# Performance work log

Measured on AMD Instinct MI355X. Metric: run time of the kernel, lower is better.

The kernel has to match this reference:

```python
import jax, jax.numpy as jnp
import numpy as np

T = 2048          # tokens (flattened batch*seq, vLLM style)
HID = 2048        # hidden_size
NH = 16           # num_heads
D_NOPE = 128
D_ROPE = 64
D_QK = D_NOPE + D_ROPE   # 192
D_V = 128
Q_LORA = 1536
KV_LORA = 512
THETA = 10000.0
EPS = 1e-6
SCALING = D_QK ** -0.5


def _rmsnorm(x, g):
    return x * jax.lax.rsqrt(jnp.mean(x * x, axis=-1, keepdims=True) + EPS) * g


def _rope(pos, x):
    # interleaved (is_neox_style=False) rotary embedding
    d = x.shape[-1]
    inv = 1.0 / (THETA ** (jnp.arange(0, d, 2, dtype=jnp.float32) / d))
    f = pos.astype(jnp.float32)[:, None] * inv          # [T, d/2]
    cos, sin = jnp.cos(f), jnp.sin(f)
    for _ in range(x.ndim - 2):                          # broadcast over heads
        cos, sin = cos[:, None], sin[:, None]
    x1, x2 = x[..., 0::2], x[..., 1::2]
    o1 = x1 * cos - x2 * sin
    o2 = x1 * sin + x2 * cos
    return jnp.stack([o1, o2], axis=-1).reshape(x.shape)


def setup_inputs() -> dict:
    key = jax.random.key(0)
    ks = jax.random.split(key, 6)
    s = 0.02
    return {
        "hidden_states": jax.random.normal(ks[0], (T, HID), jnp.float32),
        "positions": jnp.arange(T, dtype=jnp.int32),
        "w_qkv_a": jax.random.normal(ks[1], (HID, Q_LORA + KV_LORA + D_ROPE), jnp.float32) * s,
        "g_q": jnp.ones((Q_LORA,), jnp.float32),
        "w_q_b": jax.random.normal(ks[2], (Q_LORA, NH * D_QK), jnp.float32) * s,
        "g_kv": jnp.ones((KV_LORA,), jnp.float32),
        "w_kv_b": jax.random.normal(ks[3], (KV_LORA, NH * (D_NOPE + D_V)), jnp.float32) * s,
        "w_o": jax.random.normal(ks[4], (NH * D_V, HID), jnp.float32) * s,
    }


def reference(hidden_states, positions, w_qkv_a, g_q, w_q_b, g_kv, w_kv_b, w_o):
    # fused low-rank a-projection: [T, q_lora + kv_lora + rope]
    qkv_a = hidden_states @ w_qkv_a
    q_lat = qkv_a[:, :Q_LORA]
    kv_lat = qkv_a[:, Q_LORA:Q_LORA + KV_LORA]
    k_pe = qkv_a[:, Q_LORA + KV_LORA:]                   # [T, rope]

    # query path: rmsnorm -> b-projection -> [T, H, d_qk]
    q = (_rmsnorm(q_lat, g_q) @ w_q_b).reshape(T, NH, D_QK)
    q_nope, q_pe = q[..., :D_NOPE], q[..., D_NOPE:]

    # kv path: rmsnorm -> b-projection -> [T, H, nope + v]
    kv = (_rmsnorm(kv_lat, g_kv) @ w_kv_b).reshape(T, NH, D_NOPE + D_V)
    k_nope, v = kv[..., :D_NOPE], kv[..., D_NOPE:]

    q_pe = _rope(positions, q_pe)                        # [T, H, rope]
    k_pe = _rope(positions, k_pe)                        # [T, rope] shared MQA rope key

    qf = jnp.concatenate([q_nope, q_pe], axis=-1)        # [T, H, d_qk]
    kf = jnp.concatenate([k_nope, jnp.broadcast_to(k_pe[:, None, :], (T, NH, D_ROPE))], axis=-1)

    scores = jnp.einsum("thd,shd->hts", qf, kf) * SCALING   # [H, T, T]
    mask = jnp.tril(jnp.ones((T, T), dtype=bool))
    scores = jnp.where(mask, scores, jnp.finfo(scores.dtype).min)
    probs = jax.nn.softmax(scores, axis=-1)
    out = jnp.einsum("hts,shd->thd", probs, v)           # [T, H, d_v]
    return out.reshape(T, NH * D_V) @ w_o                # [T, hidden]
```

## Files before the change

### kernel.cpp

```cpp
#include <hip/hip_runtime.h>
#include <hip/hip_bf16.h>
#include <math.h>

typedef __bf16 bf16_t;
typedef __bf16 bf16x8 __attribute__((ext_vector_type(8)));
typedef float floatx4 __attribute__((ext_vector_type(4)));
typedef int intx4 __attribute__((ext_vector_type(4)));

#define T_TOK 2048
#define HID 2048
#define NH 16
#define D_NOPE 128
#define D_ROPE 64
#define D_QK 192
#define D_V 128
#define Q_LORA 1536
#define KV_LORA 512
#define QKV_N 2112
#define QKV_NPAD 2176
#define SCALING 0.07216878364870323f
#define LOG2E 1.442695041f
#define EXP_C1 (SCALING * LOG2E)
#define EXP_C2 (12.0f * LOG2E)

#define MFMA_BF16(a, b, c) __builtin_amdgcn_mfma_f32_16x16x32_bf16(a, b, c, 0, 0, 0)

__device__ __forceinline__ void gload16(const void* g, void* l) {
    __builtin_amdgcn_global_load_lds(
        (const __attribute__((address_space(1))) unsigned int*)g,
        (__attribute__((address_space(3))) unsigned int*)l, 16, 0, 0);
}

template <int MODE>
__device__ __forceinline__ void gemm_body(
    const bf16_t* __restrict__ A, const bf16_t* __restrict__ Bt,
    float* __restrict__ Cf, bf16_t* __restrict__ Cb,
    bf16_t* __restrict__ kfull, bf16_t* __restrict__ vT,
    float* __restrict__ sqq, float* __restrict__ sqkv,
    int N, int K, int Ast, int Bst, int m0, int n0, bf16_t* S)
{
    bf16_t* As = S;
    bf16_t* Bs = S + 16384;
    const int tid = threadIdx.x;
    const int lane = tid & 63;
    const int w = tid >> 6;
    const int wm = w >> 1, wn = w & 1;
    const int l15 = lane & 15, quad = lane >> 4;
    const int ckey = (l15 >> 1) & 3;

    floatx4 acc[4][4] = {};

#define GSTAGE(db_, k0_)                                                                 \
    do {                                                                                 \
        _Pragma("unroll")                                                                \
        for (int it = 0; it < 4; ++it) {                                                 \
            int slot = it * 256 + tid;                                                   \
            int kk2 = slot >> 9;                                                         \
            int r = (slot >> 2) & 127;                                                   \
            int c = slot & 3;                                                            \
            int cs = c ^ ((r >> 1) & 3);                                                 \
            gload16((const char*)(A + (size_t)(m0 + r) * Ast + (k0_) + kk2 * 32 + cs * 8),\
                    (char*)(As + (size_t)(db_)*8192) + slot * 16);                       \
            gload16((const char*)(Bt + (size_t)(n0 + r) * Bst + (k0_) + kk2 * 32 + cs * 8),\
                    (char*)(Bs + (size_t)(db_)*8192) + slot * 16);                       \
        }                                                                                \
    } while (0)

    GSTAGE(0, 0);
    int db = 0;
    for (int k0 = 0; k0 < K; k0 += 64) {
        __syncthreads();
        if (k0 + 64 < K) GSTAGE(db ^ 1, k0 + 64);
        const bf16_t* Ab = As + (size_t)db * 8192;
        const bf16_t* Bb = Bs + (size_t)db * 8192;
#pragma unroll
        for (int kk2 = 0; kk2 < 2; ++kk2) {
            bf16x8 af[4], bfr[4];
#pragma unroll
            for (int mi = 0; mi < 4; ++mi)
                af[mi] = *(const bf16x8*)(Ab + kk2 * 4096 +
                                          (wm * 64 + mi * 16 + l15) * 32 +
                                          (quad ^ ckey) * 8);
#pragma unroll
            for (int ni = 0; ni < 4; ++ni)
                bfr[ni] = *(const bf16x8*)(Bb + kk2 * 4096 +
                                           (wn * 64 + ni * 16 + l15) * 32 +
                                           (quad ^ ckey) * 8);
#pragma unroll
            for (int mi = 0; mi < 4; ++mi)
#pragma unroll
                for (int ni = 0; ni < 4; ++ni)
                    acc[mi][ni] = MFMA_BF16(af[mi], bfr[ni], acc[mi][ni]);
        }
        db ^= 1;
    }
#undef GSTAGE

    if (MODE == 3) {
#pragma unroll
        for (int mi = 0; mi < 4; ++mi)
#pragma unroll
            for (int ni = 0; ni < 4; ++ni)
#pragma unroll
                for (int r = 0; r < 4; ++r) {
                    int row = m0 + wm * 64 + mi * 16 + quad * 4 + r;
                    int col = n0 + wn * 64 + ni * 16 + l15;
                    Cb[(size_t)row * N + col] = (bf16_t)acc[mi][ni][r];
                }
        float* sq = (n0 + 128 <= Q_LORA) ? sqq
                  : ((n0 >= Q_LORA && n0 + 128 <= Q_LORA + KV_LORA) ? sqkv : nullptr);
        if (sq) {
#pragma unroll
            for (int mi = 0; mi < 4; ++mi)
#pragma unroll
                for (int r = 0; r < 4; ++r) {
                    float s = 0.f;
#pragma unroll
                    for (int ni = 0; ni < 4; ++ni) {
                        float v = acc[mi][ni][r]; s += v * v;
                    }
                    s += __shfl_xor(s, 1); s += __shfl_xor(s, 2);
                    s += __shfl_xor(s, 4); s += __shfl_xor(s, 8);
                    if (l15 == 0)
                        atomicAdd(&sq[m0 + wm * 64 + mi * 16 + quad * 4 + r], s);
                }
        }
        return;
    }

    if (MODE == 1) {
#pragma unroll
        for (int mi = 0; mi < 4; ++mi)
#pragma unroll
            for (int r = 0; r < 4; ++r) {
                int row = m0 + wm * 64 + mi * 16 + quad * 4 + r;
                float rq = rsqrtf(sqq[row] * (1.f / Q_LORA) + 1e-6f);
#pragma unroll
                for (int ni = 0; ni < 4; ++ni) {
                    int col = n0 + wn * 64 + ni * 16 + l15;
                    Cb[(size_t)row * N + col] = (bf16_t)(acc[mi][ni][r] * rq);
                }
            }
        return;
    }

    if (MODE == 2) {
        const int hh = n0 >> 8;
        if ((n0 & 255) == 0) {
#pragma unroll
            for (int mi = 0; mi < 4; ++mi)
#pragma unroll
                for (int r = 0; r < 4; ++r) {
                    int row = m0 + wm * 64 + mi * 16 + quad * 4 + r;
                    float rkv = rsqrtf(sqkv[row] * (1.f / KV_LORA) + 1e-6f);
#pragma unroll
                    for (int ni = 0; ni < 4; ++ni) {
                        int dd = wn * 64 + ni * 16 + l15;
                        kfull[((size_t)hh * T_TOK + row) * 192 + dd] =
                            (bf16_t)(acc[mi][ni][r] * rkv);
                    }
                }
        } else {
            __syncthreads();
            bf16_t* Tq = S;
#pragma unroll
            for (int mi = 0; mi < 4; ++mi)
#pragma unroll
                for (int r = 0; r < 4; ++r) {
                    int rloc = wm * 64 + mi * 16 + quad * 4 + r;
                    float rkv = rsqrtf(sqkv[m0 + rloc] * (1.f / KV_LORA) + 1e-6f);
#pragma unroll
                    for (int ni = 0; ni < 4; ++ni) {
                        int cloc = wn * 64 + ni * 16 + l15;
                        Tq[cloc * 136 + rloc] = (bf16_t)(acc[mi][ni][r] * rkv);
                    }
                }
            __syncthreads();
#pragma unroll
            for (int pass = 0; pass < 8; ++pass) {
                int dcol = pass * 16 + w * 4 + quad;
                bf16x8 vv = *(const bf16x8*)(Tq + dcol * 136 + l15 * 8);
                *(bf16x8*)(vT + ((size_t)hh * 128 + dcol) * T_TOK + m0 + l15 * 8) = vv;
            }
        }
        return;
    }

#pragma unroll
    for (int mi = 0; mi < 4; ++mi)
#pragma unroll
        for (int ni = 0; ni < 4; ++ni)
#pragma unroll
            for (int r = 0; r < 4; ++r) {
                int row = m0 + wm * 64 + mi * 16 + quad * 4 + r;
                int col = n0 + wn * 64 + ni * 16 + l15;
                Cf[(size_t)row * N + col] = acc[mi][ni][r];
            }
}

__global__ __launch_bounds__(256) void gemm_qkv_a(
    const bf16_t* __restrict__ hbf, const bf16_t* __restrict__ wt,
    bf16_t* __restrict__ qkv_ab, float* __restrict__ sqq, float* __restrict__ sqkv)
{
    __shared__ __align__(16) bf16_t S[4 * 8192];
    gemm_body<3>(hbf, wt, nullptr, qkv_ab, nullptr, nullptr, sqq, sqkv,
                 QKV_NPAD, HID, HID, HID, blockIdx.y * 128, blockIdx.x * 128, S);
}

__global__ __launch_bounds__(256) void gemm_dual(
    const bf16_t* __restrict__ qkv_ab, const bf16_t* __restrict__ wqb,
    bf16_t* __restrict__ qbuf, const bf16_t* __restrict__ wkvb,
    bf16_t* __restrict__ kfull, bf16_t* __restrict__ vT,
    float* __restrict__ sqq, float* __restrict__ sqkv)
{
    __shared__ __align__(16) bf16_t S[4 * 8192];
    int id = blockIdx.x;
    if (id < 384) {
        gemm_body<1>(qkv_ab, wqb, nullptr, qbuf, nullptr, nullptr, sqq, nullptr,
                     3072, Q_LORA, QKV_NPAD, Q_LORA,
                     (id / 24) * 128, (id % 24) * 128, S);
    } else {
        int i2 = id - 384;
        gemm_body<2>(qkv_ab + Q_LORA, wkvb, nullptr, nullptr, kfull, vT,
                     nullptr, sqkv,
                     4096, KV_LORA, QKV_NPAD, KV_LORA,
                     (i2 / 32) * 128, (i2 % 32) * 128, S);
    }
}

__global__ __launch_bounds__(256) void gemm_out(
    const bf16_t* __restrict__ attn_o, const bf16_t* __restrict__ wto,
    float* __restrict__ out)
{
    __shared__ __align__(16) bf16_t S[4 * 8192];
    gemm_body<0>(attn_o, wto, out, nullptr, nullptr, nullptr, nullptr, nullptr,
                 HID, HID, HID, HID, blockIdx.y * 128, blockIdx.x * 128, S);
}

__global__ void transpose_all(const float* __restrict__ w0, const float* __restrict__ w1,
                              const float* __restrict__ w2, const float* __restrict__ w3,
                              const float* __restrict__ hidden,
                              const float* __restrict__ g_q, const float* __restrict__ g_kv,
                              bf16_t* __restrict__ o0, bf16_t* __restrict__ o1,
                              bf16_t* __restrict__ o2, bf16_t* __restrict__ o3,
                              bf16_t* __restrict__ hbf, float* __restrict__ sqbuf) {
    int n0 = blockIdx.x * 32, k0 = blockIdx.y * 32;
    int tx = threadIdx.x, ty = threadIdx.y;
    if (blockIdx.z == 4) {
        if (blockIdx.x == 0 && blockIdx.y == 0) {
            int t = ty * 32 + tx;
            for (int j = t; j < 4096; j += 256) sqbuf[j] = 0.f;
        }
        if (n0 >= 2048 || k0 >= 2048) return;
        for (int i = ty; i < 32; i += 8)
            hbf[(size_t)(k0 + i) * 2048 + n0 + tx] =
                (bf16_t)hidden[(size_t)(k0 + i) * 2048 + n0 + tx];
        return;
    }
    const float* in; bf16_t* out; const float* g; int K, N;
    switch (blockIdx.z) {
        case 0: in = w0; out = o0; g = nullptr; K = 2048; N = 2112; break;
        case 1: in = w1; out = o1; g = g_q;     K = 1536; N = 3072; break;
        case 2: in = w2; out = o2; g = g_kv;    K = 512;  N = 4096; break;
        default: in = w3; out = o3; g = nullptr; K = 2048; N = 2048; break;
    }
    if (n0 >= N || k0 >= K) return;
    __shared__ float tile[32][33];
    for (int i = ty; i < 32; i += 8)
        tile[i][tx] = in[(size_t)(k0 + i) * N + n0 + tx];
    __syncthreads();
    float gk = g ? g[k0 + tx] : 1.f;
    for (int i = ty; i < 32; i += 8)
        out[(size_t)(n0 + i) * K + k0 + tx] = (bf16_t)(tile[tx][i] * gk);
}

__global__ void mid_fuse_lite(const bf16_t* __restrict__ qkv_ab,
                              const int* __restrict__ pos,
                              float2* __restrict__ ropet, bf16_t* __restrict__ kfull) {
    int t = blockIdx.x, tid = threadIdx.x;
    if (tid >= 32) return;
    int i = tid;
    double inv = pow(10000.0, -(double)(2 * i) / 64.0);
    double fd = (double)pos[t] * inv;
    float c = (float)cos(fd), s = (float)sin(fd);
    ropet[t * 32 + i] = make_float2(c, s);
    float x1 = (float)qkv_ab[(size_t)t * QKV_NPAD + Q_LORA + KV_LORA + 2 * i];
    float x2 = (float)qkv_ab[(size_t)t * QKV_NPAD + Q_LORA + KV_LORA + 2 * i + 1];
    bf16_t v0 = (bf16_t)(x1 * c - x2 * s);
    bf16_t v1 = (bf16_t)(x1 * s + x2 * c);
#pragma unroll
    for (int h = 0; h < NH; ++h) {
        kfull[((size_t)h * T_TOK + t) * 192 + 128 + 2 * i] = v0;
        kfull[((size_t)h * T_TOK + t) * 192 + 128 + 2 * i + 1] = v1;
    }
}

__global__ __launch_bounds__(256, 2) void attn_part(
    const bf16_t* __restrict__ qbuf, const bf16_t* __restrict__ kfull,
    const bf16_t* __restrict__ vT, const float2* __restrict__ ropet,
    bf16_t* __restrict__ oP0, bf16_t* __restrict__ oP1, float* __restrict__ l_part)
{
    const int id = blockIdx.x;
    const int h = id & 15;
    const int c = (id >> 4) & 3;
    const int qt = 15 - (id >> 6);
    const int q0 = qt * 128;
    const int nTile = 2 * (qt + 1);
    const int tbase = nTile >> 2, trem = nTile & 3;
    const int sz = tbase + (c < trem ? 1 : 0);
    const int sBeg = c * tbase + (c < trem ? c : trem);
    const int sEnd = sBeg + sz;
    const int unit = qt * 16 + h;
    const int tid = threadIdx.x, lane = tid & 63, w = tid >> 6;
    const int l15 = lane & 15, quad = lane >> 4;
    const int ckey = (l15 >> 1) & 3;

    __shared__ __align__(16) bf16_t kn2[2][6 * 64 * 32];
    __shared__ __align__(16) bf16_t vt2[2 * 128 * 32];
    __shared__ __align__(16) bf16_t p_s[128 * 64];

    bf16x8 qf[2][6];
#pragma unroll
    for (int st = 0; st < 2; ++st) {
        const bf16_t* qp = qbuf + (size_t)(q0 + w * 32 + st * 16 + l15) * (NH * D_QK) +
                           h * D_QK;
#pragma unroll
        for (int kk = 0; kk < 6; ++kk)
            qf[st][kk] = *(const bf16x8*)(qp + kk * 32 + quad * 8);
    }
#pragma unroll
    for (int st = 0; st < 2; ++st) {
        int t = q0 + w * 32 + st * 16 + l15;
#pragma unroll
        for (int kk = 4; kk < 6; ++kk)
#pragma unroll
            for (int p = 0; p < 4; ++p) {
                float2 cs = ropet[t * 32 + (kk - 4) * 16 + quad * 4 + p];
                float x1 = (float)qf[st][kk][2 * p], x2 = (float)qf[st][kk][2 * p + 1];
                qf[st][kk][2 * p] = (bf16_t)(x1 * cs.x - x2 * cs.y);
                qf[st][kk][2 * p + 1] = (bf16_t)(x1 * cs.y + x2 * cs.x);
            }
    }

    bf16x8 ones;
#pragma unroll
    for (int j = 0; j < 8; ++j) ones[j] = (bf16_t)1.0f;

    floatx4 o[2][8] = {};
    floatx4 lac[2] = {};
    intx4 vreg[4];

#define STAGE_KN(buf_, s0_)                                                              \
    do {                                                                                 \
        _Pragma("unroll")                                                                \
        for (int it = 0; it < 6; ++it) {                                                 \
            int slot = it * 256 + tid;                                                   \
            int kk = slot >> 8, s = (slot >> 2) & 63, cc = slot & 3;                     \
            int cs = cc ^ ((s >> 1) & 3);                                                \
            gload16((const char*)(kfull + ((size_t)h * T_TOK + (s0_) + s) * 192 +        \
                                  kk * 32 + cs * 8),                                     \
                    (char*)kn2[buf_] + slot * 16);                                       \
        }                                                                                \
    } while (0)

#define VLOAD(s0_)                                                                       \
    do {                                                                                 \
        _Pragma("unroll")                                                                \
        for (int it = 0; it < 4; ++it) {                                                 \
            int slot = it * 256 + tid;                                                   \
            int ks = slot >> 9, d = (slot >> 2) & 127, cc = slot & 3;                    \
            vreg[it] = *(const intx4*)(vT + ((size_t)h * 128 + d) * T_TOK + (s0_) +      \
                                       ks * 32 + cc * 8);                                \
        }                                                                                \
    } while (0)

#define VWRITE()                                                                         \
    do {                                                                                 \
        _Pragma("unroll")                                                                \
        for (int it = 0; it < 4; ++it) {                                                 \
            int slot = it * 256 + tid;                                                   \
            int ks = slot >> 9, d = (slot >> 2) & 127, cc = slot & 3;                    \
            *(intx4*)((char*)vt2 +                                                       \
                      (size_t)((ks * 512 + d * 4 + (cc ^ ((d >> 1) & 3))) * 16)) =       \
                vreg[it];                                                                \
        }                                                                                \
    } while (0)

    if (sz > 0) {
        VLOAD(sBeg * 64);
        STAGE_KN(0, sBeg * 64);
        VWRITE();
    }

    for (int si = sBeg; si < sEnd; ++si) {
        const int s0 = si * 64;
        const int buf = (si - sBeg) & 1;
        __syncthreads();
        if (si + 1 < sEnd) {
            VLOAD(s0 + 64);
            STAGE_KN(buf ^ 1, s0 + 64);
        }

        floatx4 s_acc[2][4] = {};
        __builtin_amdgcn_s_setprio(1);
#pragma unroll
        for (int ni = 0; ni < 4; ++ni) {
#pragma unroll
            for (int kk = 0; kk < 6; ++kk) {
                bf16x8 b = *(const bf16x8*)(kn2[buf] + kk * 2048 +
                                            (ni * 16 + l15) * 32 + (quad ^ ckey) * 8);
                s_acc[0][ni] = MFMA_BF16(qf[0][kk], b, s_acc[0][ni]);
                s_acc[1][ni] = MFMA_BF16(qf[1][kk], b, s_acc[1][ni]);
            }
        }
        __builtin_amdgcn_s_setprio(0);

        const bool diag = (si >= 2 * qt);
#pragma unroll
        for (int st = 0; st < 2; ++st)
#pragma unroll
            for (int ni = 0; ni < 4; ++ni)
#pragma unroll
                for (int r = 0; r < 4; ++r) {
                    int prow = w * 32 + st * 16 + quad * 4 + r;
                    int pcol = ni * 16 + l15;
                    float pv = exp2f(s_acc[st][ni][r] * EXP_C1 - EXP_C2);
                    if (diag && (s0 + pcol) > (q0 + prow)) pv = 0.f;
                    p_s[prow * 64 + ((((pcol >> 3) ^ (prow & 7))) << 3) + (pcol & 7)] =
                        (bf16_t)pv;
                }

        __builtin_amdgcn_s_setprio(1);
#pragma unroll
        for (int ks = 0; ks < 2; ++ks) {
            bf16x8 a0, a1;
            {
                int arow = w * 32 + l15;
                a0 = *(const bf16x8*)(p_s + arow * 64 +
                                      (((ks * 4 + quad) ^ (arow & 7)) << 3));
                arow += 16;
                a1 = *(const bf16x8*)(p_s + arow * 64 +
                                      (((ks * 4 + quad) ^ (arow & 7)) << 3));
            }
            lac[0] = MFMA_BF16(a0, ones, lac[0]);
            lac[1] = MFMA_BF16(a1, ones, lac[1]);
#pragma unroll
            for (int ni = 0; ni < 8; ++ni) {
                bf16x8 b = *(const bf16x8*)(vt2 + ks * 4096 +
                                            (ni * 16 + l15) * 32 + (quad ^ ckey) * 8);
                o[0][ni] = MFMA_BF16(a0, b, o[0][ni]);
                o[1][ni] = MFMA_BF16(a1, b, o[1][ni]);
            }
        }
        __builtin_amdgcn_s_setprio(0);

        __syncthreads();
        if (si + 1 < sEnd) VWRITE();
    }

    bf16_t* op = ((c < 2) ? oP0 : oP1) + (size_t)(unit * 2 + (c & 1)) * 128 * 128;
#pragma unroll
    for (int st = 0; st < 2; ++st) {
#pragma unroll
        for (int ni = 0; ni < 8; ++ni)
#pragma unroll
            for (int r = 0; r < 4; ++r) {
                int lrow = w * 32 + st * 16 + quad * 4 + r;
                op[(size_t)lrow * 128 + ni * 16 + l15] = (bf16_t)o[st][ni][r];
            }
        if (l15 == 0)
#pragma unroll
            for (int r = 0; r < 4; ++r) {
                int lrow = w * 32 + st * 16 + quad * 4 + r;
                l_part[((size_t)unit * 4 + c) * 128 + lrow] = lac[st][r];
            }
    }
#undef STAGE_KN
#undef VLOAD
#undef VWRITE
}

__global__ void attn_combine(const bf16_t* __restrict__ oP0,
                             const bf16_t* __restrict__ oP1,
                             const float* __restrict__ l_part,
                             bf16_t* __restrict__ attn_o)
{
    int idx = blockIdx.x * 256 + threadIdx.x;
    int t = idx >> 8, cg = idx & 255;
    int col = cg * 8;
    int h = col >> 7, d = col & 127;
    int qt = t >> 7, lrow = t & 127;
    size_t unit = (size_t)qt * 16 + h;
    const float* lp = l_part + unit * 4 * 128 + lrow;
    float inv = 1.f / (lp[0] + lp[128] + lp[256] + lp[384]);
    size_t r0 = ((unit * 2 + 0) * 128 + lrow) * 128 + d;
    size_t r1 = ((unit * 2 + 1) * 128 + lrow) * 128 + d;
    bf16x8 a0 = *(const bf16x8*)(oP0 + r0);
    bf16x8 a1 = *(const bf16x8*)(oP0 + r1);
    bf16x8 a2 = *(const bf16x8*)(oP1 + r0);
    bf16x8 a3 = *(const bf16x8*)(oP1 + r1);
    bf16x8 out;
#pragma unroll
    for (int j = 0; j < 8; ++j)
        out[j] = (bf16_t)(((float)a0[j] + (float)a1[j] + (float)a2[j] + (float)a3[j]) * inv);
    *(bf16x8*)(attn_o + (size_t)t * (NH * D_V) + col) = out;
}

extern "C" void kernel_launch(void* const* d_in, const int* in_sizes, int n_in,
                              void* d_out, int out_size, void* d_ws, size_t ws_size,
                              hipStream_t stream) {
    const float* hidden = (const float*)d_in[0];
    const int* positions = (const int*)d_in[1];
    const float* w_qkv_a = (const float*)d_in[2];
    const float* g_q = (const float*)d_in[3];
    const float* w_q_b = (const float*)d_in[4];
    const float* g_kv = (const float*)d_in[5];
    const float* w_kv_b = (const float*)d_in[6];
    const float* w_o = (const float*)d_in[7];
    float* out = (float*)d_out;

    char* p = (char*)d_ws;
    bf16_t* qkv_ab = (bf16_t*)p;
    bf16_t* attn_o = (bf16_t*)p;
    p += (size_t)T_TOK * QKV_NPAD * 4;
    bf16_t* hbf = (bf16_t*)p;
    p += (size_t)T_TOK * HID * 2;
    bf16_t* qbuf = (bf16_t*)p;  p += (size_t)T_TOK * NH * D_QK * 2;
    bf16_t* vtmp = (bf16_t*)p;  p += (size_t)T_TOK * NH * D_V * 2;
    bf16_t* kfull = (bf16_t*)p; p += (size_t)NH * T_TOK * 192 * 2;
    bf16_t* vT = (bf16_t*)p;    p += (size_t)NH * 128 * T_TOK * 2;
    bf16_t* wt_qkv_a = (bf16_t*)p; p += (size_t)QKV_NPAD * HID * 2;
    bf16_t* wt_q_b = (bf16_t*)p;   p += (size_t)3072 * Q_LORA * 2;
    bf16_t* wt_kv_b = (bf16_t*)p;  p += (size_t)4096 * KV_LORA * 2;
    bf16_t* wt_o = (bf16_t*)p;

    float2* ropet = (float2*)vtmp;
    float* l_part = (float*)((char*)vtmp + (1 << 20));
    float* sq_q = (float*)((char*)vtmp + (2 << 20));
    float* sq_kv = sq_q + 2048;
    bf16_t* oP0 = wt_qkv_a;
    bf16_t* oP1 = (bf16_t*)((char*)d_ws + (size_t)T_TOK * HID * 2);

    dim3 tb(32, 8);

    transpose_all<<<dim3(128, 64, 5), tb, 0, stream>>>(
        w_qkv_a, w_q_b, w_kv_b, w_o, hidden, g_q, g_kv,
        wt_qkv_a, wt_q_b, wt_kv_b, wt_o, hbf, sq_q);

    gemm_qkv_a<<<dim3(QKV_NPAD / 128, T_TOK / 128), 256, 0, stream>>>(
        hbf, wt_qkv_a, qkv_ab, sq_q, sq_kv);

    mid_fuse_lite<<<T_TOK, 64, 0, stream>>>(qkv_ab, positions, ropet, kfull);

    gemm_dual<<<896, 256, 0, stream>>>(qkv_ab, wt_q_b, qbuf, wt_kv_b, kfull, vT,
                                       sq_q, sq_kv);

    attn_part<<<1024, 256, 0, stream>>>(qbuf, kfull, vT, ropet, oP0, oP1, l_part);
    attn_combine<<<(T_TOK * 256) / 256, 256, 0, stream>>>(oP0, oP1, l_part, attn_o);

    gemm_out<<<dim3(HID / 128, T_TOK / 128), 256, 0, stream>>>(attn_o, wt_o, out);
}
```

Measured before the change: 302.6 us.

## Single-buffer K tile and split P staging to fit three attention blocks per CU

Drops the double-buffered K shared-memory tile in favour of a single buffer. The next tile's K staging and V register load now start only after the QK MFMAs finish and a barrier is passed. The P tile is halved to 64x32 and is written and consumed per 32-column k-slice inside the PV loop, with a new swizzle. The LDS savings, together with launch bounds raised from 2 to 3 blocks, are meant to raise occupancy. In exchange it loses the within-block prefetch overlap of K loads with compute, and the tighter register cap risks spills.

```diff
diff --git a/kernel.cpp b/kernel.cpp
--- a/kernel.cpp
+++ b/kernel.cpp
@@ -295,7 +295,7 @@
     }
 }
 
-__global__ __launch_bounds__(256, 2) void attn_part(
+__global__ __launch_bounds__(256, 3) void attn_part(
     const bf16_t* __restrict__ qbuf, const bf16_t* __restrict__ kfull,
     const bf16_t* __restrict__ vT, const float2* __restrict__ ropet,
     bf16_t* __restrict__ oP0, bf16_t* __restrict__ oP1, float* __restrict__ l_part)
@@ -315,9 +315,9 @@
     const int l15 = lane & 15, quad = lane >> 4;
     const int ckey = (l15 >> 1) & 3;
 
-    __shared__ __align__(16) bf16_t kn2[2][6 * 64 * 32];
+    __shared__ __align__(16) bf16_t kn[6 * 64 * 32];
     __shared__ __align__(16) bf16_t vt2[2 * 128 * 32];
-    __shared__ __align__(16) bf16_t p_s[128 * 64];
+    __shared__ __align__(16) bf16_t p_s[128 * 32];
 
     bf16x8 qf[2][6];
 #pragma unroll
@@ -350,7 +350,7 @@
     floatx4 lac[2] = {};
     intx4 vreg[4];
 
-#define STAGE_KN(buf_, s0_)                                                              \
+#define STAGE_KN(s0_)                                                                    \
     do {                                                                                 \
         _Pragma("unroll")                                                                \
         for (int it = 0; it < 6; ++it) {                                                 \
@@ -359,7 +359,7 @@
             int cs = cc ^ ((s >> 1) & 3);                                                \
             gload16((const char*)(kfull + ((size_t)h * T_TOK + (s0_) + s) * 192 +        \
                                   kk * 32 + cs * 8),                                     \
-                    (char*)kn2[buf_] + slot * 16);                                       \
+                    (char*)kn + slot * 16);                                              \
         }                                                                                \
     } while (0)
 
@@ -387,19 +387,14 @@
     } while (0)
 
     if (sz > 0) {
+        STAGE_KN(sBeg * 64);
         VLOAD(sBeg * 64);
-        STAGE_KN(0, sBeg * 64);
         VWRITE();
     }
 
     for (int si = sBeg; si < sEnd; ++si) {
         const int s0 = si * 64;
-        const int buf = (si - sBeg) & 1;
         __syncthreads();
-        if (si + 1 < sEnd) {
-            VLOAD(s0 + 64);
-            STAGE_KN(buf ^ 1, s0 + 64);
-        }
 
         floatx4 s_acc[2][4] = {};
         __builtin_amdgcn_s_setprio(1);
@@ -407,7 +402,7 @@
         for (int ni = 0; ni < 4; ++ni) {
 #pragma unroll
             for (int kk = 0; kk < 6; ++kk) {
-                bf16x8 b = *(const bf16x8*)(kn2[buf] + kk * 2048 +
+                bf16x8 b = *(const bf16x8*)(kn + kk * 2048 +
                                             (ni * 16 + l15) * 32 + (quad ^ ckey) * 8);
                 s_acc[0][ni] = MFMA_BF16(qf[0][kk], b, s_acc[0][ni]);
                 s_acc[1][ni] = MFMA_BF16(qf[1][kk], b, s_acc[1][ni]);
@@ -415,32 +410,37 @@
         }
         __builtin_amdgcn_s_setprio(0);
 
+        __syncthreads();
+        if (si + 1 < sEnd) {
+            STAGE_KN(s0 + 64);
+            VLOAD(s0 + 64);
+        }
+
         const bool diag = (si >= 2 * qt);
 #pragma unroll
-        for (int st = 0; st < 2; ++st)
-#pragma unroll
-            for (int ni = 0; ni < 4; ++ni)
-#pragma unroll
-                for (int r = 0; r < 4; ++r) {
-                    int prow = w * 32 + st * 16 + quad * 4 + r;
-                    int pcol = ni * 16 + l15;
-                    float pv = exp2f(s_acc[st][ni][r] * EXP_C1 - EXP_C2);
-                    if (diag && (s0 + pcol) > (q0 + prow)) pv = 0.f;
-                    p_s[prow * 64 + ((((pcol >> 3) ^ (prow & 7))) << 3) + (pcol & 7)] =
-                        (bf16_t)pv;
-                }
-
-        __builtin_amdgcn_s_setprio(1);
-#pragma unroll
         for (int ks = 0; ks < 2; ++ks) {
+#pragma unroll
+            for (int st = 0; st < 2; ++st)
+#pragma unroll
+                for (int nl = 0; nl < 2; ++nl)
+#pragma unroll
+                    for (int r = 0; r < 4; ++r) {
+                        int prow = w * 32 + st * 16 + quad * 4 + r;
+                        int cloc = nl * 16 + l15;
+                        float pv = exp2f(s_acc[st][ks * 2 + nl][r] * EXP_C1 - EXP_C2);
+                        if (diag && (s0 + ks * 32 + cloc) > (q0 + prow)) pv = 0.f;
+                        p_s[prow * 32 + ((((cloc >> 3) ^ ((prow >> 1) & 3))) << 3) +
+                            (cloc & 7)] = (bf16_t)pv;
+                    }
+            __builtin_amdgcn_s_setprio(1);
             bf16x8 a0, a1;
             {
                 int arow = w * 32 + l15;
-                a0 = *(const bf16x8*)(p_s + arow * 64 +
-                                      (((ks * 4 + quad) ^ (arow & 7)) << 3));
+                a0 = *(const bf16x8*)(p_s + arow * 32 +
+                                      ((quad ^ ((arow >> 1) & 3)) << 3));
                 arow += 16;
-                a1 = *(const bf16x8*)(p_s + arow * 64 +
-                                      (((ks * 4 + quad) ^ (arow & 7)) << 3));
+                a1 = *(const bf16x8*)(p_s + arow * 32 +
+                                      ((quad ^ ((arow >> 1) & 3)) << 3));
             }
             lac[0] = MFMA_BF16(a0, ones, lac[0]);
             lac[1] = MFMA_BF16(a1, ones, lac[1]);
@@ -451,8 +451,8 @@
                 o[0][ni] = MFMA_BF16(a0, b, o[0][ni]);
                 o[1][ni] = MFMA_BF16(a1, b, o[1][ni]);
             }
-        }
-        __builtin_amdgcn_s_setprio(0);
+            __builtin_amdgcn_s_setprio(0);
+        }
 
         __syncthreads();
         if (si + 1 < sEnd) VWRITE();
```

Result: slower. 391.4 us (+29.4%).
